# Optimization experiments

Hardware: AMD Instinct MI355X
Metric: run time of the kernel (lower is better)

Reference implementation:

```python
import jax, jax.numpy as jnp
import numpy as np

B, N, D, H = 8, 1024, 512, 8
HEAD_DIM = D // H


def setup_inputs() -> dict:
    key = jax.random.key(0)
    k1, k2, k3, k4 = jax.random.split(key, 4)
    x = jax.random.normal(k1, (B, N, D), dtype=jnp.float32)
    relative_bias_logits = jax.random.normal(k2, (B, N, N, H), dtype=jnp.float32)
    # Dense params (fan-in scaled like lecun init)
    W_qkv = jax.random.normal(k3, (D, 3 * D), dtype=jnp.float32) / np.sqrt(D)
    b_qkv = jnp.zeros((3 * D,), dtype=jnp.float32)
    W_o = jax.random.normal(k4, (D, D), dtype=jnp.float32) / np.sqrt(D)
    b_o = jnp.zeros((D,), dtype=jnp.float32)
    return {"x": x, "relative_bias_logits": relative_bias_logits,
            "W_qkv": W_qkv, "b_qkv": b_qkv, "W_o": W_o, "b_o": b_o}


def reference(x, relative_bias_logits, W_qkv, b_qkv, W_o, b_o):
    # x: (B, N, D); relative_bias_logits: (B, N, N, H)
    n_heads = relative_bias_logits.shape[-1]
    emb = x.shape[-1]
    head_dim = emb // n_heads
    n = x.shape[-2]
    batch_dim = x.shape[:-2]

    qkv = x @ W_qkv + b_qkv                                   # (B, N, 3D)
    qkv = qkv.reshape(*batch_dim, n, n_heads, 3, head_dim)    # (B, N, H, 3, T)
    q, k, v = qkv[..., 0, :], qkv[..., 1, :], qkv[..., 2, :]  # each (B, N, H, T)

    logits = jnp.einsum('...QHT,...KHT->...QKH', q, k) / jnp.sqrt(
        jnp.asarray(head_dim, dtype=x.dtype))
    logits = logits + relative_bias_logits                    # (B, Q, K, H)
    # softmax over the K axis (axis=-2); jax.nn.softmax is max-stable
    attention = jax.nn.softmax(logits, axis=-2)
    # dropout deterministic (train=False): identity
    y = jnp.einsum('...QKH,...KHT->...QHT', attention, v)     # (B, N, H, T)
    y = y.reshape(*batch_dim, n, emb)                          # (B, N, D)
    y = y @ W_o + b_o
    return y
```

## Files before the change

### kernel.cpp

```cpp
#include <hip/hip_runtime.h>

typedef unsigned short u16;
typedef __attribute__((ext_vector_type(8))) short short8;
typedef __attribute__((ext_vector_type(4))) float f32x4;

__device__ __forceinline__ u16 f2bf(float f) {
  union { float f; unsigned u; } c; c.f = f;
  unsigned u = c.u;
  return (u16)((u + 0x7FFFu + ((u >> 16) & 1u)) >> 16);
}

__global__ __launch_bounds__(256) void cvt_x_kernel(const float* __restrict__ x,
                                                    u16* __restrict__ xb) {
  int i = blockIdx.x * 256 + threadIdx.x;
  float4 v = ((const float4*)x)[i];
  uint2 st;
  st.x = (unsigned)f2bf(v.x) | ((unsigned)f2bf(v.y) << 16);
  st.y = (unsigned)f2bf(v.z) | ((unsigned)f2bf(v.w) << 16);
  ((uint2*)xb)[i] = st;
}

__global__ __launch_bounds__(256) void transp_kernel(const float* __restrict__ W,
                                                     u16* __restrict__ Wt,
                                                     int NC, int total) {
  int idx = blockIdx.x * 256 + threadIdx.x;
  if (idx >= total) return;
  int n = idx >> 9, k = idx & 511;
  Wt[idx] = f2bf(W[(size_t)k * NC + n]);
}

template<int MODE>
__global__ __launch_bounds__(256) void gemm_kernel(
    const u16* __restrict__ A, const u16* __restrict__ Bt,
    const float* __restrict__ biasv,
    u16* __restrict__ qb, u16* __restrict__ kb, u16* __restrict__ vtb,
    float* __restrict__ outp) {
  __shared__ u16 As[64 * 64];
  __shared__ u16 Bs[64 * 64];
  const int tid = threadIdx.x;
  const int lane = tid & 63;
  const int w = tid >> 6, wm = w >> 1, wn = w & 1;
  const int m0 = blockIdx.y * 64, n0 = blockIdx.x * 64;
  const int r = tid >> 3, s = tid & 7;
  const int lm = lane & 15, lg = lane >> 4;
  f32x4 acc[2][2] = {};

  for (int k0 = 0; k0 < 512; k0 += 64) {
    __syncthreads();
    *(uint4*)&As[r * 64 + s * 8]        = *(const uint4*)&A[(size_t)(m0 + r) * 512 + k0 + s * 8];
    *(uint4*)&As[(r + 32) * 64 + s * 8] = *(const uint4*)&A[(size_t)(m0 + r + 32) * 512 + k0 + s * 8];
    *(uint4*)&Bs[r * 64 + s * 8]        = *(const uint4*)&Bt[(size_t)(n0 + r) * 512 + k0 + s * 8];
    *(uint4*)&Bs[(r + 32) * 64 + s * 8] = *(const uint4*)&Bt[(size_t)(n0 + r + 32) * 512 + k0 + s * 8];
    __syncthreads();
#pragma unroll
    for (int tc = 0; tc < 2; tc++) {
      short8 bfr[2];
#pragma unroll
      for (int nt = 0; nt < 2; nt++)
        bfr[nt] = *(const short8*)&Bs[(wn * 32 + nt * 16 + lm) * 64 + tc * 32 + lg * 8];
#pragma unroll
      for (int mt = 0; mt < 2; mt++) {
        short8 af = *(const short8*)&As[(wm * 32 + mt * 16 + lm) * 64 + tc * 32 + lg * 8];
#pragma unroll
        for (int nt = 0; nt < 2; nt++)
          acc[mt][nt] = __builtin_amdgcn_mfma_f32_16x16x32_bf16(af, bfr[nt], acc[mt][nt], 0, 0, 0);
      }
    }
  }

#pragma unroll
  for (int mt = 0; mt < 2; mt++) {
#pragma unroll
    for (int nt = 0; nt < 2; nt++) {
      const int col = n0 + wn * 32 + nt * 16 + lm;
      const float bv = biasv[col];
#pragma unroll
      for (int r2 = 0; r2 < 4; r2++) {
        const int row = m0 + wm * 32 + mt * 16 + lg * 4 + r2;
        const float v = acc[mt][nt][r2] + bv;
        if (MODE == 0) {
          const int h = col / 192, rem = col % 192;
          const int which = rem >> 6, t = rem & 63;
          const int b = row >> 10, n = row & 1023;
          const u16 bb = f2bf(v);
          if (which == 0)      qb[((size_t)(b * 8 + h) * 1024 + n) * 64 + t] = bb;
          else if (which == 1) kb[((size_t)(b * 8 + h) * 1024 + n) * 64 + t] = bb;
          else                 vtb[((size_t)(b * 8 + h) * 64 + t) * 1024 + n] = bb;
        } else {
          outp[(size_t)row * 512 + col] = v;
        }
      }
    }
  }
}

__global__ __launch_bounds__(512) void attn_kernel(
    const u16* __restrict__ qb, const u16* __restrict__ kb,
    const u16* __restrict__ vtb, const float* __restrict__ bias,
    u16* __restrict__ yb) {
  __shared__ float biasS[8 * 32 * 34];
  __shared__ u16 Ps[8 * 32 * 40];
  const int tid = threadIdx.x;
  const int lane = tid & 63;
  const int h = tid >> 6;
  const int b = blockIdx.y;
  const int q0 = blockIdx.x * 32;
  const size_t bh = (size_t)b * 8 + h;
  const u16* Q  = qb  + bh * (1024 * 64);
  const u16* K  = kb  + bh * (1024 * 64);
  const u16* VT = vtb + bh * (64 * 1024);
  const int lm = lane & 15, lg = lane >> 4;

  short8 aq[2][2];
#pragma unroll
  for (int mt = 0; mt < 2; mt++)
#pragma unroll
    for (int tc = 0; tc < 2; tc++)
      aq[mt][tc] = *(const short8*)&Q[(size_t)(q0 + mt * 16 + lm) * 64 + tc * 32 + lg * 8];

  f32x4 o[2][4] = {};
  float mrow[2][4], lrow[2][4];
#pragma unroll
  for (int mt = 0; mt < 2; mt++)
#pragma unroll
    for (int r2 = 0; r2 < 4; r2++) { mrow[mt][r2] = -1e30f; lrow[mt][r2] = 0.f; }

  const float SC   = 0.125f * 1.4426950408889634f;
  const float LG2E = 1.4426950408889634f;

  const int kl = lane >> 1, h4 = (lane & 1) * 4;
  float4 pre[4];
#pragma unroll
  for (int rr = 0; rr < 4; rr++) {
    const int qr = h + rr * 8;
    pre[rr] = *(const float4*)&bias[(((size_t)(b * 1024 + q0 + qr)) * 1024 + kl) * 8 + h4];
  }

  for (int kc = 0; kc < 1024; kc += 32) {
    __syncthreads();
#pragma unroll
    for (int rr = 0; rr < 4; rr++) {
      const int qr = h + rr * 8;
      biasS[(h4 + 0) * 1088 + qr * 34 + kl] = pre[rr].x;
      biasS[(h4 + 1) * 1088 + qr * 34 + kl] = pre[rr].y;
      biasS[(h4 + 2) * 1088 + qr * 34 + kl] = pre[rr].z;
      biasS[(h4 + 3) * 1088 + qr * 34 + kl] = pre[rr].w;
    }
    __syncthreads();
    if (kc + 32 < 1024) {
#pragma unroll
      for (int rr = 0; rr < 4; rr++) {
        const int qr = h + rr * 8;
        pre[rr] = *(const float4*)&bias[(((size_t)(b * 1024 + q0 + qr)) * 1024 + (kc + 32) + kl) * 8 + h4];
      }
    }

    f32x4 sf[2][2];
#pragma unroll
    for (int kt = 0; kt < 2; kt++) {
      short8 bk[2];
#pragma unroll
      for (int tc = 0; tc < 2; tc++)
        bk[tc] = *(const short8*)&K[(size_t)(kc + kt * 16 + lm) * 64 + tc * 32 + lg * 8];
#pragma unroll
      for (int mt = 0; mt < 2; mt++) {
        f32x4 c = {0.f, 0.f, 0.f, 0.f};
        c = __builtin_amdgcn_mfma_f32_16x16x32_bf16(aq[mt][0], bk[0], c, 0, 0, 0);
        c = __builtin_amdgcn_mfma_f32_16x16x32_bf16(aq[mt][1], bk[1], c, 0, 0, 0);
        sf[mt][kt] = c;
      }
    }

#pragma unroll
    for (int mt = 0; mt < 2; mt++) {
      float pv2[2][4];
      const int qrb = mt * 16 + lg * 4;
#pragma unroll
      for (int kt = 0; kt < 2; kt++)
#pragma unroll
        for (int r2 = 0; r2 < 4; r2++)
          pv2[kt][r2] = sf[mt][kt][r2] * SC +
                        biasS[h * 1088 + (qrb + r2) * 34 + kt * 16 + lm] * LG2E;
      float rmax[4];
#pragma unroll
      for (int r2 = 0; r2 < 4; r2++) rmax[r2] = fmaxf(pv2[0][r2], pv2[1][r2]);
#pragma unroll
      for (int d = 1; d < 16; d <<= 1)
#pragma unroll
        for (int r2 = 0; r2 < 4; r2++)
          rmax[r2] = fmaxf(rmax[r2], __shfl_xor(rmax[r2], d));
      float alpha[4];
#pragma unroll
      for (int r2 = 0; r2 < 4; r2++) {
        const float mn = fmaxf(mrow[mt][r2], rmax[r2]);
        alpha[r2] = exp2f(mrow[mt][r2] - mn);
        mrow[mt][r2] = mn;
      }
      float rsum[4] = {0.f, 0.f, 0.f, 0.f};
#pragma unroll
      for (int kt = 0; kt < 2; kt++)
#pragma unroll
        for (int r2 = 0; r2 < 4; r2++) {
          const float p = exp2f(pv2[kt][r2] - mrow[mt][r2]);
          pv2[kt][r2] = p;
          rsum[r2] += p;
        }
#pragma unroll
      for (int d = 1; d < 16; d <<= 1)
#pragma unroll
        for (int r2 = 0; r2 < 4; r2++)
          rsum[r2] += __shfl_xor(rsum[r2], d);
#pragma unroll
      for (int r2 = 0; r2 < 4; r2++)
        lrow[mt][r2] = lrow[mt][r2] * alpha[r2] + rsum[r2];
#pragma unroll
      for (int nt = 0; nt < 4; nt++)
#pragma unroll
        for (int r2 = 0; r2 < 4; r2++)
          o[mt][nt][r2] *= alpha[r2];
#pragma unroll
      for (int kt = 0; kt < 2; kt++)
#pragma unroll
        for (int r2 = 0; r2 < 4; r2++)
          Ps[h * 1280 + (qrb + r2) * 40 + kt * 16 + lm] = f2bf(pv2[kt][r2]);
    }

    short8 bv[4];
#pragma unroll
    for (int nt = 0; nt < 4; nt++)
      bv[nt] = *(const short8*)&VT[(size_t)(nt * 16 + lm) * 1024 + kc + lg * 8];
#pragma unroll
    for (int mt = 0; mt < 2; mt++) {
      short8 ap = *(const short8*)&Ps[h * 1280 + (mt * 16 + lm) * 40 + lg * 8];
#pragma unroll
      for (int nt = 0; nt < 4; nt++)
        o[mt][nt] = __builtin_amdgcn_mfma_f32_16x16x32_bf16(ap, bv[nt], o[mt][nt], 0, 0, 0);
    }
  }

#pragma unroll
  for (int mt = 0; mt < 2; mt++)
#pragma unroll
    for (int nt = 0; nt < 4; nt++)
#pragma unroll
      for (int r2 = 0; r2 < 4; r2++) {
        const int row = q0 + mt * 16 + lg * 4 + r2;
        const float yv = o[mt][nt][r2] / lrow[mt][r2];
        yb[((size_t)(b * 1024 + row)) * 512 + h * 64 + nt * 16 + lm] = f2bf(yv);
      }
}

extern "C" void kernel_launch(void* const* d_in, const int* in_sizes, int n_in,
                              void* d_out, int out_size, void* d_ws, size_t ws_size,
                              hipStream_t stream) {
  const float* x    = (const float*)d_in[0];
  const float* bias = (const float*)d_in[1];
  const float* Wqkv = (const float*)d_in[2];
  const float* bqkv = (const float*)d_in[3];
  const float* Wo   = (const float*)d_in[4];
  const float* bo   = (const float*)d_in[5];
  float* out = (float*)d_out;

  char* p = (char*)d_ws;
  u16* xb    = (u16*)p; p += (size_t)8192 * 512 * 2;
  u16* wqkvT = (u16*)p; p += (size_t)1536 * 512 * 2;
  u16* woT   = (u16*)p; p += (size_t)512 * 512 * 2;
  u16* qB    = (u16*)p; p += (size_t)8 * 8 * 1024 * 64 * 2;
  u16* kB    = (u16*)p; p += (size_t)8 * 8 * 1024 * 64 * 2;
  u16* vtB   = (u16*)p; p += (size_t)8 * 8 * 64 * 1024 * 2;
  u16* yB    = (u16*)p; p += (size_t)8192 * 512 * 2;

  cvt_x_kernel<<<4096, 256, 0, stream>>>(x, xb);
  transp_kernel<<<3072, 256, 0, stream>>>(Wqkv, wqkvT, 1536, 1536 * 512);
  transp_kernel<<<1024, 256, 0, stream>>>(Wo, woT, 512, 512 * 512);
  gemm_kernel<0><<<dim3(24, 128), 256, 0, stream>>>(xb, wqkvT, bqkv, qB, kB, vtB, nullptr);
  attn_kernel<<<dim3(32, 8), 512, 0, stream>>>(qB, kB, vtB, bias, yB);
  gemm_kernel<1><<<dim3(8, 128), 256, 0, stream>>>(yB, woT, bo, nullptr, nullptr, nullptr, out);
}
```

Measured before the change: 512.0 us.

## Rework GEMM tiling with LDS direct loads, tiled transpose, and restructured attention

The weight transpose now goes through a shared-memory tile so both reads and writes are coalesced. The GEMMs switch to 128-row tiles with global_load_lds direct-to-LDS copies. The attention kernel halves its query tile to 16 rows, which doubles the grid to 512 blocks for better occupancy. It also double-buffers the bias in LDS to remove one barrier per iteration, skips the rescale when the running max does not change, defers the row-sum reduction to the end, and adds s_setprio around the MFMAs. The risks are the LDS layout assumed by the direct loads, lower K/V reuse per block, and a data-dependent branch.

Result: slower. 531.8 us (+3.9%).

```diff
diff --git a/kernel.cpp b/kernel.cpp
--- a/kernel.cpp
+++ b/kernel.cpp
@@ -8,6 +8,12 @@
   union { float f; unsigned u; } c; c.f = f;
   unsigned u = c.u;
   return (u16)((u + 0x7FFFu + ((u >> 16) & 1u)) >> 16);
+}
+
+__device__ __forceinline__ void gload16(const u16* g, u16* l) {
+  __builtin_amdgcn_global_load_lds(
+      (const __attribute__((address_space(1))) void*)g,
+      (__attribute__((address_space(3))) void*)l, 16, 0, 0);
 }
 
 __global__ __launch_bounds__(256) void cvt_x_kernel(const float* __restrict__ x,
@@ -21,233 +27,236 @@
 }
 
 __global__ __launch_bounds__(256) void transp_kernel(const float* __restrict__ W,
-                                                     u16* __restrict__ Wt,
-                                                     int NC, int total) {
-  int idx = blockIdx.x * 256 + threadIdx.x;
-  if (idx >= total) return;
-  int n = idx >> 9, k = idx & 511;
-  Wt[idx] = f2bf(W[(size_t)k * NC + n]);
-}
-
-template<int MODE>
+                                                     u16* __restrict__ Wt, int NC) {
+  __shared__ u16 tile[32][33];
+  const int tx = threadIdx.x & 31, ty = threadIdx.x >> 5;
+  const int n0 = blockIdx.x * 32, k0 = blockIdx.y * 32;
+#pragma unroll
+  for (int i = 0; i < 4; i++)
+    tile[ty + i * 8][tx] = f2bf(W[(size_t)(k0 + ty + i * 8) * NC + n0 + tx]);
+  __syncthreads();
+#pragma unroll
+  for (int i = 0; i < 4; i++)
+    Wt[(size_t)(n0 + ty + i * 8) * 512 + k0 + tx] = tile[tx][ty + i * 8];
+}
+
+template<int MODE, int BN>
 __global__ __launch_bounds__(256) void gemm_kernel(
     const u16* __restrict__ A, const u16* __restrict__ Bt,
     const float* __restrict__ biasv,
     u16* __restrict__ qb, u16* __restrict__ kb, u16* __restrict__ vtb,
     float* __restrict__ outp) {
-  __shared__ u16 As[64 * 64];
-  __shared__ u16 Bs[64 * 64];
+  constexpr int BM = 128;
+  constexpr int NI = BN / 32;
+  __shared__ u16 As[BM * 64];
+  __shared__ u16 Bs[BN * 64];
   const int tid = threadIdx.x;
   const int lane = tid & 63;
   const int w = tid >> 6, wm = w >> 1, wn = w & 1;
-  const int m0 = blockIdx.y * 64, n0 = blockIdx.x * 64;
-  const int r = tid >> 3, s = tid & 7;
+  const int m0 = blockIdx.y * BM, n0 = blockIdx.x * BN;
   const int lm = lane & 15, lg = lane >> 4;
-  f32x4 acc[2][2] = {};
+  const int sr = tid >> 3, sc = (tid & 7) * 8;
+  f32x4 acc[4][NI] = {};
 
   for (int k0 = 0; k0 < 512; k0 += 64) {
     __syncthreads();
-    *(uint4*)&As[r * 64 + s * 8]        = *(const uint4*)&A[(size_t)(m0 + r) * 512 + k0 + s * 8];
-    *(uint4*)&As[(r + 32) * 64 + s * 8] = *(const uint4*)&A[(size_t)(m0 + r + 32) * 512 + k0 + s * 8];
-    *(uint4*)&Bs[r * 64 + s * 8]        = *(const uint4*)&Bt[(size_t)(n0 + r) * 512 + k0 + s * 8];
-    *(uint4*)&Bs[(r + 32) * 64 + s * 8] = *(const uint4*)&Bt[(size_t)(n0 + r + 32) * 512 + k0 + s * 8];
+#pragma unroll
+    for (int c = 0; c < BM / 32; c++)
+      gload16(&A[(size_t)(m0 + sr + c * 32) * 512 + k0 + sc], &As[c * 2048 + w * 512]);
+#pragma unroll
+    for (int c = 0; c < BN / 32; c++)
+      gload16(&Bt[(size_t)(n0 + sr + c * 32) * 512 + k0 + sc], &Bs[c * 2048 + w * 512]);
     __syncthreads();
 #pragma unroll
     for (int tc = 0; tc < 2; tc++) {
-      short8 bfr[2];
-#pragma unroll
-      for (int nt = 0; nt < 2; nt++)
-        bfr[nt] = *(const short8*)&Bs[(wn * 32 + nt * 16 + lm) * 64 + tc * 32 + lg * 8];
-#pragma unroll
-      for (int mt = 0; mt < 2; mt++) {
-        short8 af = *(const short8*)&As[(wm * 32 + mt * 16 + lm) * 64 + tc * 32 + lg * 8];
-#pragma unroll
-        for (int nt = 0; nt < 2; nt++)
-          acc[mt][nt] = __builtin_amdgcn_mfma_f32_16x16x32_bf16(af, bfr[nt], acc[mt][nt], 0, 0, 0);
-      }
-    }
-  }
-
-#pragma unroll
-  for (int mt = 0; mt < 2; mt++) {
-#pragma unroll
-    for (int nt = 0; nt < 2; nt++) {
-      const int col = n0 + wn * 32 + nt * 16 + lm;
+      short8 bf[NI];
+#pragma unroll
+      for (int ni = 0; ni < NI; ni++)
+        bf[ni] = *(const short8*)&Bs[(wn * (BN / 2) + ni * 16 + lm) * 64 + tc * 32 + lg * 8];
+#pragma unroll
+      for (int mi = 0; mi < 4; mi++) {
+        short8 af = *(const short8*)&As[(wm * 64 + mi * 16 + lm) * 64 + tc * 32 + lg * 8];
+#pragma unroll
+        for (int ni = 0; ni < NI; ni++)
+          acc[mi][ni] = __builtin_amdgcn_mfma_f32_16x16x32_bf16(af, bf[ni], acc[mi][ni], 0, 0, 0);
+      }
+    }
+  }
+
+#pragma unroll
+  for (int mi = 0; mi < 4; mi++)
+#pragma unroll
+    for (int ni = 0; ni < NI; ni++) {
+      const int col = n0 + wn * (BN / 2) + ni * 16 + lm;
       const float bv = biasv[col];
 #pragma unroll
       for (int r2 = 0; r2 < 4; r2++) {
-        const int row = m0 + wm * 32 + mt * 16 + lg * 4 + r2;
-        const float v = acc[mt][nt][r2] + bv;
+        const int row = m0 + wm * 64 + mi * 16 + lg * 4 + r2;
+        const float v = acc[mi][ni][r2] + bv;
         if (MODE == 0) {
-          const int h = col / 192, rem = col % 192;
+          const int hh = col / 192, rem = col % 192;
           const int which = rem >> 6, t = rem & 63;
           const int b = row >> 10, n = row & 1023;
           const u16 bb = f2bf(v);
-          if (which == 0)      qb[((size_t)(b * 8 + h) * 1024 + n) * 64 + t] = bb;
-          else if (which == 1) kb[((size_t)(b * 8 + h) * 1024 + n) * 64 + t] = bb;
-          else                 vtb[((size_t)(b * 8 + h) * 64 + t) * 1024 + n] = bb;
+          if (which == 0)      qb[((size_t)(b * 8 + hh) * 1024 + n) * 64 + t] = bb;
+          else if (which == 1) kb[((size_t)(b * 8 + hh) * 1024 + n) * 64 + t] = bb;
+          else                 vtb[((size_t)(b * 8 + hh) * 64 + t) * 1024 + n] = bb;
         } else {
           outp[(size_t)row * 512 + col] = v;
         }
       }
     }
-  }
-}
-
-__global__ __launch_bounds__(512) void attn_kernel(
+}
+
+__global__ __launch_bounds__(512, 4) void attn_kernel(
     const u16* __restrict__ qb, const u16* __restrict__ kb,
     const u16* __restrict__ vtb, const float* __restrict__ bias,
     u16* __restrict__ yb) {
-  __shared__ float biasS[8 * 32 * 34];
-  __shared__ u16 Ps[8 * 32 * 40];
+  __shared__ float biasS[2 * 8 * 16 * 34];
+  __shared__ u16 Ps[8 * 16 * 40];
   const int tid = threadIdx.x;
   const int lane = tid & 63;
   const int h = tid >> 6;
   const int b = blockIdx.y;
-  const int q0 = blockIdx.x * 32;
+  const int q0 = blockIdx.x * 16;
   const size_t bh = (size_t)b * 8 + h;
   const u16* Q  = qb  + bh * (1024 * 64);
   const u16* K  = kb  + bh * (1024 * 64);
   const u16* VT = vtb + bh * (64 * 1024);
   const int lm = lane & 15, lg = lane >> 4;
 
-  short8 aq[2][2];
-#pragma unroll
-  for (int mt = 0; mt < 2; mt++)
-#pragma unroll
-    for (int tc = 0; tc < 2; tc++)
-      aq[mt][tc] = *(const short8*)&Q[(size_t)(q0 + mt * 16 + lm) * 64 + tc * 32 + lg * 8];
-
-  f32x4 o[2][4] = {};
-  float mrow[2][4], lrow[2][4];
-#pragma unroll
-  for (int mt = 0; mt < 2; mt++)
-#pragma unroll
-    for (int r2 = 0; r2 < 4; r2++) { mrow[mt][r2] = -1e30f; lrow[mt][r2] = 0.f; }
+  short8 aq[2];
+#pragma unroll
+  for (int tc = 0; tc < 2; tc++)
+    aq[tc] = *(const short8*)&Q[(size_t)(q0 + lm) * 64 + tc * 32 + lg * 8];
+
+  f32x4 o[4] = {};
+  float mrow[4], psum[4];
+#pragma unroll
+  for (int r2 = 0; r2 < 4; r2++) { mrow[r2] = -1e30f; psum[r2] = 0.f; }
 
   const float SC   = 0.125f * 1.4426950408889634f;
   const float LG2E = 1.4426950408889634f;
 
   const int kl = lane >> 1, h4 = (lane & 1) * 4;
-  float4 pre[4];
-#pragma unroll
-  for (int rr = 0; rr < 4; rr++) {
+  const size_t brow = (size_t)(b * 1024 + q0);
+
+#pragma unroll
+  for (int rr = 0; rr < 2; rr++) {
     const int qr = h + rr * 8;
-    pre[rr] = *(const float4*)&bias[(((size_t)(b * 1024 + q0 + qr)) * 1024 + kl) * 8 + h4];
-  }
-
-  for (int kc = 0; kc < 1024; kc += 32) {
-    __syncthreads();
-#pragma unroll
-    for (int rr = 0; rr < 4; rr++) {
-      const int qr = h + rr * 8;
-      biasS[(h4 + 0) * 1088 + qr * 34 + kl] = pre[rr].x;
-      biasS[(h4 + 1) * 1088 + qr * 34 + kl] = pre[rr].y;
-      biasS[(h4 + 2) * 1088 + qr * 34 + kl] = pre[rr].z;
-      biasS[(h4 + 3) * 1088 + qr * 34 + kl] = pre[rr].w;
-    }
-    __syncthreads();
-    if (kc + 32 < 1024) {
-#pragma unroll
-      for (int rr = 0; rr < 4; rr++) {
+    float4 p0 = *(const float4*)&bias[((brow + qr) * 1024 + kl) * 8 + h4];
+    biasS[(h4 + 0) * 544 + qr * 34 + kl] = p0.x;
+    biasS[(h4 + 1) * 544 + qr * 34 + kl] = p0.y;
+    biasS[(h4 + 2) * 544 + qr * 34 + kl] = p0.z;
+    biasS[(h4 + 3) * 544 + qr * 34 + kl] = p0.w;
+  }
+  __syncthreads();
+
+  for (int it = 0; it < 32; it++) {
+    const int kc = it * 32;
+    const int bb = (it & 1) * 4352;
+
+    float4 pre[2];
+    const bool havePre = (it < 31);
+    if (havePre) {
+#pragma unroll
+      for (int rr = 0; rr < 2; rr++) {
         const int qr = h + rr * 8;
-        pre[rr] = *(const float4*)&bias[(((size_t)(b * 1024 + q0 + qr)) * 1024 + (kc + 32) + kl) * 8 + h4];
-      }
-    }
-
-    f32x4 sf[2][2];
+        pre[rr] = *(const float4*)&bias[((brow + qr) * 1024 + kc + 32 + kl) * 8 + h4];
+      }
+    }
+
+    f32x4 sf[2];
+    __builtin_amdgcn_s_setprio(1);
 #pragma unroll
     for (int kt = 0; kt < 2; kt++) {
-      short8 bk[2];
-#pragma unroll
-      for (int tc = 0; tc < 2; tc++)
-        bk[tc] = *(const short8*)&K[(size_t)(kc + kt * 16 + lm) * 64 + tc * 32 + lg * 8];
-#pragma unroll
-      for (int mt = 0; mt < 2; mt++) {
-        f32x4 c = {0.f, 0.f, 0.f, 0.f};
-        c = __builtin_amdgcn_mfma_f32_16x16x32_bf16(aq[mt][0], bk[0], c, 0, 0, 0);
-        c = __builtin_amdgcn_mfma_f32_16x16x32_bf16(aq[mt][1], bk[1], c, 0, 0, 0);
-        sf[mt][kt] = c;
-      }
-    }
-
-#pragma unroll
-    for (int mt = 0; mt < 2; mt++) {
-      float pv2[2][4];
-      const int qrb = mt * 16 + lg * 4;
-#pragma unroll
-      for (int kt = 0; kt < 2; kt++)
-#pragma unroll
-        for (int r2 = 0; r2 < 4; r2++)
-          pv2[kt][r2] = sf[mt][kt][r2] * SC +
-                        biasS[h * 1088 + (qrb + r2) * 34 + kt * 16 + lm] * LG2E;
-      float rmax[4];
-#pragma unroll
-      for (int r2 = 0; r2 < 4; r2++) rmax[r2] = fmaxf(pv2[0][r2], pv2[1][r2]);
-#pragma unroll
-      for (int d = 1; d < 16; d <<= 1)
-#pragma unroll
-        for (int r2 = 0; r2 < 4; r2++)
-          rmax[r2] = fmaxf(rmax[r2], __shfl_xor(rmax[r2], d));
-      float alpha[4];
-#pragma unroll
-      for (int r2 = 0; r2 < 4; r2++) {
-        const float mn = fmaxf(mrow[mt][r2], rmax[r2]);
-        alpha[r2] = exp2f(mrow[mt][r2] - mn);
-        mrow[mt][r2] = mn;
-      }
-      float rsum[4] = {0.f, 0.f, 0.f, 0.f};
-#pragma unroll
-      for (int kt = 0; kt < 2; kt++)
-#pragma unroll
-        for (int r2 = 0; r2 < 4; r2++) {
-          const float p = exp2f(pv2[kt][r2] - mrow[mt][r2]);
-          pv2[kt][r2] = p;
-          rsum[r2] += p;
-        }
-#pragma unroll
-      for (int d = 1; d < 16; d <<= 1)
-#pragma unroll
-        for (int r2 = 0; r2 < 4; r2++)
-          rsum[r2] += __shfl_xor(rsum[r2], d);
-#pragma unroll
-      for (int r2 = 0; r2 < 4; r2++)
-        lrow[mt][r2] = lrow[mt][r2] * alpha[r2] + rsum[r2];
-#pragma unroll
-      for (int nt = 0; nt < 4; nt++)
-#pragma unroll
-        for (int r2 = 0; r2 < 4; r2++)
-          o[mt][nt][r2] *= alpha[r2];
-#pragma unroll
-      for (int kt = 0; kt < 2; kt++)
-#pragma unroll
-        for (int r2 = 0; r2 < 4; r2++)
-          Ps[h * 1280 + (qrb + r2) * 40 + kt * 16 + lm] = f2bf(pv2[kt][r2]);
-    }
+      short8 bk0 = *(const short8*)&K[(size_t)(kc + kt * 16 + lm) * 64 + lg * 8];
+      short8 bk1 = *(const short8*)&K[(size_t)(kc + kt * 16 + lm) * 64 + 32 + lg * 8];
+      f32x4 c = {0.f, 0.f, 0.f, 0.f};
+      c = __builtin_amdgcn_mfma_f32_16x16x32_bf16(aq[0], bk0, c, 0, 0, 0);
+      c = __builtin_amdgcn_mfma_f32_16x16x32_bf16(aq[1], bk1, c, 0, 0, 0);
+      sf[kt] = c;
+    }
+    __builtin_amdgcn_s_setprio(0);
 
     short8 bv[4];
 #pragma unroll
     for (int nt = 0; nt < 4; nt++)
       bv[nt] = *(const short8*)&VT[(size_t)(nt * 16 + lm) * 1024 + kc + lg * 8];
-#pragma unroll
-    for (int mt = 0; mt < 2; mt++) {
-      short8 ap = *(const short8*)&Ps[h * 1280 + (mt * 16 + lm) * 40 + lg * 8];
-#pragma unroll
-      for (int nt = 0; nt < 4; nt++)
-        o[mt][nt] = __builtin_amdgcn_mfma_f32_16x16x32_bf16(ap, bv[nt], o[mt][nt], 0, 0, 0);
-    }
-  }
-
-#pragma unroll
-  for (int mt = 0; mt < 2; mt++)
+
+    float pv2[2][4];
+#pragma unroll
+    for (int kt = 0; kt < 2; kt++)
+#pragma unroll
+      for (int r2 = 0; r2 < 4; r2++)
+        pv2[kt][r2] = sf[kt][r2] * SC +
+                      biasS[bb + h * 544 + (lg * 4 + r2) * 34 + kt * 16 + lm] * LG2E;
+    float rmax[4];
+#pragma unroll
+    for (int r2 = 0; r2 < 4; r2++) rmax[r2] = fmaxf(pv2[0][r2], pv2[1][r2]);
+#pragma unroll
+    for (int d = 1; d < 16; d <<= 1)
+#pragma unroll
+      for (int r2 = 0; r2 < 4; r2++)
+        rmax[r2] = fmaxf(rmax[r2], __shfl_xor(rmax[r2], d));
+    const float g = fmaxf(fmaxf(rmax[0] - mrow[0], rmax[1] - mrow[1]),
+                          fmaxf(rmax[2] - mrow[2], rmax[3] - mrow[3]));
+    if (!__all(g <= 0.f)) {
+#pragma unroll
+      for (int r2 = 0; r2 < 4; r2++) {
+        const float mn = fmaxf(mrow[r2], rmax[r2]);
+        const float al = exp2f(mrow[r2] - mn);
+        mrow[r2] = mn;
+        psum[r2] *= al;
+#pragma unroll
+        for (int nt = 0; nt < 4; nt++) o[nt][r2] *= al;
+      }
+    }
+#pragma unroll
+    for (int kt = 0; kt < 2; kt++)
+#pragma unroll
+      for (int r2 = 0; r2 < 4; r2++) {
+        const float p = exp2f(pv2[kt][r2] - mrow[r2]);
+        psum[r2] += p;
+        Ps[h * 640 + (lg * 4 + r2) * 40 + kt * 16 + lm] = f2bf(p);
+      }
+
+    short8 ap = *(const short8*)&Ps[h * 640 + lm * 40 + lg * 8];
+    __builtin_amdgcn_s_setprio(1);
 #pragma unroll
     for (int nt = 0; nt < 4; nt++)
-#pragma unroll
-      for (int r2 = 0; r2 < 4; r2++) {
-        const int row = q0 + mt * 16 + lg * 4 + r2;
-        const float yv = o[mt][nt][r2] / lrow[mt][r2];
-        yb[((size_t)(b * 1024 + row)) * 512 + h * 64 + nt * 16 + lm] = f2bf(yv);
-      }
+      o[nt] = __builtin_amdgcn_mfma_f32_16x16x32_bf16(ap, bv[nt], o[nt], 0, 0, 0);
+    __builtin_amdgcn_s_setprio(0);
+
+    if (havePre) {
+      const int nb = ((it + 1) & 1) * 4352;
+#pragma unroll
+      for (int rr = 0; rr < 2; rr++) {
+        const int qr = h + rr * 8;
+        biasS[nb + (h4 + 0) * 544 + qr * 34 + kl] = pre[rr].x;
+        biasS[nb + (h4 + 1) * 544 + qr * 34 + kl] = pre[rr].y;
+        biasS[nb + (h4 + 2) * 544 + qr * 34 + kl] = pre[rr].z;
+        biasS[nb + (h4 + 3) * 544 + qr * 34 + kl] = pre[rr].w;
+      }
+      __syncthreads();
+    }
+  }
+
+  float lr[4];
+#pragma unroll
+  for (int r2 = 0; r2 < 4; r2++) {
+    float s = psum[r2];
+#pragma unroll
+    for (int d = 1; d < 16; d <<= 1) s += __shfl_xor(s, d);
+    lr[r2] = s;
+  }
+#pragma unroll
+  for (int nt = 0; nt < 4; nt++)
+#pragma unroll
+    for (int r2 = 0; r2 < 4; r2++) {
+      const int row = q0 + lg * 4 + r2;
+      yb[((size_t)(b * 1024 + row)) * 512 + h * 64 + nt * 16 + lm] = f2bf(o[nt][r2] / lr[r2]);
+    }
 }
 
 extern "C" void kernel_launch(void* const* d_in, const int* in_sizes, int n_in,
@@ -271,9 +280,9 @@
   u16* yB    = (u16*)p; p += (size_t)8192 * 512 * 2;
 
   cvt_x_kernel<<<4096, 256, 0, stream>>>(x, xb);
-  transp_kernel<<<3072, 256, 0, stream>>>(Wqkv, wqkvT, 1536, 1536 * 512);
-  transp_kernel<<<1024, 256, 0, stream>>>(Wo, woT, 512, 512 * 512);
-  gemm_kernel<0><<<dim3(24, 128), 256, 0, stream>>>(xb, wqkvT, bqkv, qB, kB, vtB, nullptr);
-  attn_kernel<<<dim3(32, 8), 512, 0, stream>>>(qB, kB, vtB, bias, yB);
-  gemm_kernel<1><<<dim3(8, 128), 256, 0, stream>>>(yB, woT, bo, nullptr, nullptr, nullptr, out);
-}
+  transp_kernel<<<dim3(48, 16), 256, 0, stream>>>(Wqkv, wqkvT, 1536);
+  transp_kernel<<<dim3(16, 16), 256, 0, stream>>>(Wo, woT, 512);
+  gemm_kernel<0, 128><<<dim3(12, 64), 256, 0, stream>>>(xb, wqkvT, bqkv, qB, kB, vtB, nullptr);
+  attn_kernel<<<dim3(64, 8), 512, 0, stream>>>(qB, kB, vtB, bias, yB);
+  gemm_kernel<1, 64><<<dim3(8, 64), 256, 0, stream>>>(yB, woT, bo, nullptr, nullptr, nullptr, out);
+}
```
